# Performance work log

Hardware: AMD Instinct MI355X
Metric: run time of the kernel (lower is better)

## Reference

```python
import jax, jax.numpy as jnp
import numpy as np

H = 1024  # hidden_size
T = 64    # decode steps
B = 256
D_IN = 1024


def setup_inputs() -> dict:
    key = jax.random.key(0)
    ks = jax.random.split(key, 8)
    s = 0.05
    x = jax.random.normal(ks[0], (B, D_IN), dtype=jnp.float32)
    # first_state_dense: Dense(H, tanh)
    W_fs = jax.random.normal(ks[1], (D_IN, H), dtype=jnp.float32) * s
    b_fs = jnp.zeros((H,), dtype=jnp.float32)
    # output_dense: Dense(H, relu)
    W_out = jax.random.normal(ks[2], (H, H), dtype=jnp.float32) * s
    b_out = jnp.zeros((H,), dtype=jnp.float32)
    # Keras GRUCell (reset_after=True): kernel [H,3H], recurrent [H,3H], bias [2,3H]
    W_k = jax.random.normal(ks[3], (H, 3 * H), dtype=jnp.float32) * s
    W_r = jax.random.normal(ks[4], (H, 3 * H), dtype=jnp.float32) * s
    b_gru = jnp.zeros((2, 3 * H), dtype=jnp.float32)
    return {"x": x, "W_fs": W_fs, "b_fs": b_fs, "W_out": W_out,
            "b_out": b_out, "W_k": W_k, "W_r": W_r, "b_gru": b_gru}


def _gru_step(h, inp, W_k, W_r, b_gru):
    # Keras GRUCell math with reset_after=True (TF2 default)
    mx = inp @ W_k + b_gru[0]          # [B,3H]
    mh = h @ W_r + b_gru[1]            # [B,3H]
    xz, xr, xh = jnp.split(mx, 3, axis=-1)
    hz, hr, hh = jnp.split(mh, 3, axis=-1)
    z = jax.nn.sigmoid(xz + hz)
    r = jax.nn.sigmoid(xr + hr)
    hh_cand = jnp.tanh(xh + r * hh)
    return z * h + (1.0 - z) * hh_cand


def reference(x, W_fs, b_fs, W_out, b_out, W_k, W_r, b_gru):
    h0 = jnp.tanh(x @ W_fs + b_fs)  # [B,H]

    def step(h, _):
        out = jax.nn.relu(h @ W_out + b_out)   # [B,H]
        h_new = _gru_step(h, out, W_k, W_r, b_gru)
        return h_new, out

    h_final, outs = jax.lax.scan(step, h0, None, length=T)  # outs: [T,B,H]
    final_out = jax.nn.relu(h_final @ W_out + b_out)         # [B,H]
    # original collects T+1 outputs then drops the first
    collected = jnp.concatenate([outs[1:], final_out[None]], axis=0)  # [T,B,H]
    return jnp.transpose(collected, (1, 0, 2))  # [B,T,H]
```

## Files before the change

kernel.cpp:

```cpp
#include <hip/hip_runtime.h>
#include <math.h>

#define HDIM 1024
#define BROWS 256
#define TSTEPS 64
#define TH3 3072
#define RSCALE 1024.0f
#define RINV   0.0009765625f

typedef _Float16 half8 __attribute__((ext_vector_type(8)));
typedef float float4v __attribute__((ext_vector_type(4)));

__device__ __forceinline__ float sigmoidf_(float x) {
    return 1.0f / (1.0f + __expf(-x));
}

__device__ __forceinline__ float4v mfma16(half8 a, half8 b, float4v c) {
    return __builtin_amdgcn_mfma_f32_16x16x32_f16(a, b, c, 0, 0, 0);
}

__device__ __forceinline__ int frag_idx(int m, int k) {
    return (((m >> 4) * 32 + (k >> 5)) * 64 + ((m & 15) + (((k & 31) >> 3) << 4))) * 8 + (k & 7);
}

__device__ __forceinline__ void split16(float v, _Float16* hp, _Float16* lp) {
    const _Float16 h = (_Float16)v;
    *hp = h;
    *lp = (_Float16)((v - (float)h) * RSCALE);
}

__device__ __forceinline__ void st_h16(_Float16* p, _Float16 v) {
    const unsigned u = (unsigned)__builtin_bit_cast(unsigned short, v);
    asm volatile("global_store_short %0, %1, off sc0 sc1"
                 :: "v"(p), "v"(u) : "memory");
}

__device__ __forceinline__ void gbar_arrive(unsigned* bar, unsigned gen, bool isdes) {
    asm volatile("s_waitcnt vmcnt(0)" ::: "memory");
    __syncthreads();
    if (threadIdx.x == 0) {
        if (isdes) {
            asm volatile("buffer_inv sc0 sc1\n\ts_waitcnt vmcnt(0)" ::: "memory");
        } else {
            asm volatile("buffer_inv sc0\n\ts_waitcnt vmcnt(0)" ::: "memory");
        }
        unsigned* gc = bar + ((blockIdx.x & 7) << 5);
        unsigned* rc = bar + 256;
        const unsigned old = __hip_atomic_fetch_add(gc, 1u, __ATOMIC_RELAXED,
                                                    __HIP_MEMORY_SCOPE_AGENT);
        if (old + 1u == gen * 32u)
            __hip_atomic_fetch_add(rc, 1u, __ATOMIC_RELAXED,
                                   __HIP_MEMORY_SCOPE_AGENT);
    }
}

__device__ __forceinline__ void gbar_wait(unsigned* bar, unsigned gen) {
    if (threadIdx.x == 0) {
        unsigned* rc = bar + 256;
        while (__hip_atomic_load(rc, __ATOMIC_RELAXED,
                                 __HIP_MEMORY_SCOPE_AGENT) < gen * 8u)
            __builtin_amdgcn_s_sleep(1);
    }
    __syncthreads();
    asm volatile("" ::: "memory");
}

__device__ __forceinline__ void gbar(unsigned* bar, unsigned gen, bool isdes) {
    gbar_arrive(bar, gen, isdes);
    gbar_wait(bar, gen);
}

__device__ __forceinline__ void gbar_full(unsigned* bar, unsigned gen) {
    asm volatile("s_waitcnt vmcnt(0)" ::: "memory");
    __syncthreads();
    __builtin_amdgcn_fence(__ATOMIC_ACQUIRE, "agent");
    if (threadIdx.x == 0) {
        unsigned* gc = bar + ((blockIdx.x & 7) << 5);
        unsigned* rc = bar + 256;
        const unsigned old = __hip_atomic_fetch_add(gc, 1u, __ATOMIC_RELAXED,
                                                    __HIP_MEMORY_SCOPE_AGENT);
        if (old + 1u == gen * 32u)
            __hip_atomic_fetch_add(rc, 1u, __ATOMIC_RELAXED,
                                   __HIP_MEMORY_SCOPE_AGENT);
    }
    gbar_wait(bar, gen);
}

__device__ __forceinline__ void gemm_panel(
    const half8* __restrict__ AH, const half8* __restrict__ AL,
    const _Float16* __restrict__ WH, const _Float16* __restrict__ WL,
    int mt0, int mt1, int lane, int rot,
    float4v& aH0, float4v& aXa0, float4v& aXb0,
    float4v& aH1, float4v& aXa1, float4v& aXb1)
{
    half8 rA[2][2][4];
    const int base0 = mt0 * 2048 + lane;
    const int base1 = mt1 * 2048 + lane;
    const int lofs = lane * 8;
#pragma unroll
    for (int kk = 0; kk < 2; ++kk) {
        const int kt = (rot & 15) * 2 + kk;
        rA[0][kk][0] = AH[base0 + kt * 64];
        rA[0][kk][1] = AL[base0 + kt * 64];
        rA[0][kk][2] = AH[base1 + kt * 64];
        rA[0][kk][3] = AL[base1 + kt * 64];
    }
#pragma unroll
    for (int c = 0; c < 16; ++c) {
        if (c < 15) {
#pragma unroll
            for (int kk = 0; kk < 2; ++kk) {
                const int kt = (((c + 1) + rot) & 15) * 2 + kk;
                rA[(c + 1) & 1][kk][0] = AH[base0 + kt * 64];
                rA[(c + 1) & 1][kk][1] = AL[base0 + kt * 64];
                rA[(c + 1) & 1][kk][2] = AH[base1 + kt * 64];
                rA[(c + 1) & 1][kk][3] = AL[base1 + kt * 64];
            }
        }
#pragma unroll
        for (int kk = 0; kk < 2; ++kk) {
            const int kt = ((c + rot) & 15) * 2 + kk;
            const half8 bh = *(const half8*)&WH[kt * 512 + lofs];
            const half8 bl = *(const half8*)&WL[kt * 512 + lofs];
            const half8 a0h = rA[c & 1][kk][0];
            const half8 a0l = rA[c & 1][kk][1];
            const half8 a1h = rA[c & 1][kk][2];
            const half8 a1l = rA[c & 1][kk][3];
            aH0  = mfma16(a0h, bh, aH0);
            aXa0 = mfma16(a0l, bh, aXa0);
            aXb0 = mfma16(a0h, bl, aXb0);
            aH1  = mfma16(a1h, bh, aH1);
            aXa1 = mfma16(a1l, bh, aXa1);
            aXb1 = mfma16(a1h, bl, aXb1);
        }
    }
}

__global__ __launch_bounds__(512, 2) void decoder_mfma(
    const float* __restrict__ x,
    const float* __restrict__ W_fs, const float* __restrict__ b_fs,
    const float* __restrict__ W_out, const float* __restrict__ b_out,
    const float* __restrict__ W_k,  const float* __restrict__ W_r,
    const float* __restrict__ b_gru,
    float* __restrict__ dout,
    _Float16* __restrict__ hH, _Float16* __restrict__ hL,
    _Float16* __restrict__ oH, _Float16* __restrict__ oL,
    unsigned* __restrict__ bar)
{
    extern __shared__ _Float16 ldsh[];
    _Float16* WAh = ldsh;
    _Float16* WAl = ldsh + 16384;
    _Float16* WBh = ldsh + 32768;
    _Float16* WBl = ldsh + 49152;
    float*    mhs = (float*)(ldsh + 65536);
    volatile unsigned* peer_sh = (volatile unsigned*)(ldsh + 71680);

    const int b    = blockIdx.x;
    const int tid  = threadIdx.x;
    const int wv   = tid >> 6;
    const int lane = tid & 63;
    const int nn   = lane & 15;
    const int kq   = lane >> 4;

    unsigned xcd;
    asm("s_getreg_b32 %0, hwreg(HW_REG_XCC_ID)" : "=s"(xcd));
    xcd &= 7u;
    if (tid == 0) {
        __hip_atomic_fetch_max(&bar[288 + xcd], (unsigned)b, __ATOMIC_RELAXED,
                               __HIP_MEMORY_SCOPE_AGENT);
        peer_sh[0] = __hip_atomic_fetch_add(&bar[296 + xcd], 1u, __ATOMIC_RELAXED,
                                            __HIP_MEMORY_SCOPE_AGENT);
    }

    for (int idx = tid; idx < 16384; idx += 512) {
        const int k = idx >> 4, n = idx & 15;
        float w;
        if (n < 4) {
            w = W_out[(size_t)k * HDIM + 4 * b + n];
        } else {
            const int q = n - 4, jj = q / 3, ch = q - 3 * jj;
            w = W_r[(size_t)k * TH3 + ch * 1024 + 4 * b + jj];
        }
        const int hw = ((k >> 5) * 64 + n + (((k & 31) >> 3) << 4)) * 8 + (k & 7);
        split16(w, &WAh[hw], &WAl[hw]);
    }
    for (int idx = tid; idx < 16384; idx += 512) {
        const int k = idx >> 4, n = idx & 15;
        float w = 0.0f;
        if (n < 12) {
            const int jj = n / 3, ch = n - 3 * jj;
            w = W_k[(size_t)k * TH3 + ch * 1024 + 4 * b + jj];
        }
        const int hw = ((k >> 5) * 64 + n + (((k & 31) >> 3) << 4)) * 8 + (k & 7);
        split16(w, &WBh[hw], &WBl[hw]);
    }

    float bA;
    if (nn < 4) {
        bA = b_out[4 * b + nn];
    } else {
        const int q = nn - 4, jj = q / 3, ch = q - 3 * jj;
        bA = b_gru[TH3 + ch * 1024 + 4 * b + jj];
    }
    float bB = 0.0f;
    if (nn < 12) {
        const int jj = nn / 3, ch = nn - 3 * jj;
        bB = b_gru[ch * 1024 + 4 * b + jj];
    }

    {
        const int row = tid & 255;
        const int c = 4 * b + ((tid >> 8) << 1);
        float a0 = 0.0f, a1 = 0.0f;
        const float* xr = x + (size_t)row * HDIM;
        for (int k = 0; k < HDIM; k += 4) {
            const float4 xv = *(const float4*)(xr + k);
#pragma unroll
            for (int kk = 0; kk < 4; ++kk) {
                const float2 wv2 = *(const float2*)(W_fs + (size_t)(k + kk) * HDIM + c);
                const float av = (&xv.x)[kk];
                a0 = fmaf(av, wv2.x, a0);
                a1 = fmaf(av, wv2.y, a1);
            }
        }
        const float h0 = tanhf(a0 + b_fs[c]);
        const float h1 = tanhf(a1 + b_fs[c + 1]);
        _Float16 hi, lo;
        split16(h0, &hi, &lo);
        st_h16(&hH[frag_idx(row, c)], hi);
        st_h16(&hL[frag_idx(row, c)], lo);
        split16(h1, &hi, &lo);
        st_h16(&hH[frag_idx(row, c + 1)], hi);
        st_h16(&hL[frag_idx(row, c + 1)], lo);
    }
    unsigned gen = 0;
    gbar_full(bar, ++gen);

    const unsigned desblk = __hip_atomic_load(&bar[288 + xcd], __ATOMIC_RELAXED,
                                              __HIP_MEMORY_SCOPE_AGENT);
    const bool isdes = (desblk == (unsigned)b);
    const int p = (int)(peer_sh[0] & 31u);
    const int pair = (wv + (p & 7)) & 7;
    const int rot  = ((p >> 3) & 3) << 2;
    const int mt0 = 2 * pair, mt1 = 2 * pair + 1;
    float hreg[2][4];

    for (int t = 0; ; ++t) {
        {
            float4v aH0 = {0.f,0.f,0.f,0.f}, aXa0 = {0.f,0.f,0.f,0.f}, aXb0 = {0.f,0.f,0.f,0.f};
            float4v aH1 = {0.f,0.f,0.f,0.f}, aXa1 = {0.f,0.f,0.f,0.f}, aXb1 = {0.f,0.f,0.f,0.f};
            gemm_panel((const half8*)hH, (const half8*)hL, WAh, WAl,
                       mt0, mt1, lane, rot, aH0, aXa0, aXb0, aH1, aXa1, aXb1);
#pragma unroll
            for (int m = 0; m < 2; ++m) {
                const int mt = (m == 0) ? mt0 : mt1;
#pragma unroll
                for (int r = 0; r < 4; ++r) {
                    const int row = mt * 16 + kq * 4 + r;
                    float v = ((m == 0) ? aH0[r] + (aXa0[r] + aXb0[r]) * RINV
                                        : aH1[r] + (aXa1[r] + aXb1[r]) * RINV) + bA;
                    if (nn < 4) {
                        v = fmaxf(v, 0.0f);
                        if (t < TSTEPS) {
                            _Float16 hi, lo;
                            split16(v, &hi, &lo);
                            const int fi = frag_idx(row, 4 * b + nn);
                            st_h16(&oH[fi], hi);
                            st_h16(&oL[fi], lo);
                        }
                    } else if (t < TSTEPS) {
                        mhs[row * 12 + (nn - 4)] = v;
                    }
                }
            }
            if (t == TSTEPS) {
                if (nn < 4) {
#pragma unroll
                    for (int m = 0; m < 2; ++m) {
                        const int mt = (m == 0) ? mt0 : mt1;
#pragma unroll
                        for (int r = 0; r < 4; ++r) {
                            const int row = mt * 16 + kq * 4 + r;
                            const float v = fmaxf(((m == 0) ? aH0[r] + (aXa0[r] + aXb0[r]) * RINV
                                                            : aH1[r] + (aXa1[r] + aXb1[r]) * RINV) + bA, 0.0f);
                            __builtin_nontemporal_store(
                                v, &dout[(size_t)row * (TSTEPS * HDIM) +
                                         (size_t)(TSTEPS - 1) * HDIM + 4 * b + nn]);
                        }
                    }
                }
                break;
            }
            gbar_arrive(bar, ++gen, isdes);
            if (nn < 4 && t >= 1) {
#pragma unroll
                for (int m = 0; m < 2; ++m) {
                    const int mt = (m == 0) ? mt0 : mt1;
#pragma unroll
                    for (int r = 0; r < 4; ++r) {
                        const int row = mt * 16 + kq * 4 + r;
                        const float v = fmaxf(((m == 0) ? aH0[r] + (aXa0[r] + aXb0[r]) * RINV
                                                        : aH1[r] + (aXa1[r] + aXb1[r]) * RINV) + bA, 0.0f);
                        __builtin_nontemporal_store(
                            v, &dout[(size_t)row * (TSTEPS * HDIM) +
                                     (size_t)(t - 1) * HDIM + 4 * b + nn]);
                    }
                }
            }
            gbar_wait(bar, gen);
        }

        {
            float4v aH0 = {0.f,0.f,0.f,0.f}, aXa0 = {0.f,0.f,0.f,0.f}, aXb0 = {0.f,0.f,0.f,0.f};
            float4v aH1 = {0.f,0.f,0.f,0.f}, aXa1 = {0.f,0.f,0.f,0.f}, aXb1 = {0.f,0.f,0.f,0.f};
            gemm_panel((const half8*)oH, (const half8*)oL, WBh, WBl,
                       mt0, mt1, lane, rot, aH0, aXa0, aXb0, aH1, aXa1, aXb1);
            float vals[2][4], v1[2][4], v2[2][4];
#pragma unroll
            for (int r = 0; r < 4; ++r) {
                vals[0][r] = aH0[r] + (aXa0[r] + aXb0[r]) * RINV + bB;
                vals[1][r] = aH1[r] + (aXa1[r] + aXb1[r]) * RINV + bB;
            }
#pragma unroll
            for (int m = 0; m < 2; ++m)
#pragma unroll
                for (int r = 0; r < 4; ++r) {
                    v1[m][r] = __shfl(vals[m][r], (lane + 1) & 63);
                    v2[m][r] = __shfl(vals[m][r], (lane + 2) & 63);
                }
            if (nn < 12 && (nn % 3) == 0) {
                const int jj = nn / 3;
                const int j = 4 * b + jj;
                if (t == 0) {
#pragma unroll
                    for (int m = 0; m < 2; ++m)
#pragma unroll
                        for (int r = 0; r < 4; ++r) {
                            const int mt = (m == 0) ? mt0 : mt1;
                            const int row = mt * 16 + kq * 4 + r;
                            const int fi = frag_idx(row, j);
                            hreg[m][r] = (float)hH[fi] + (float)hL[fi] * RINV;
                        }
                }
#pragma unroll
                for (int m = 0; m < 2; ++m) {
                    const int mt = (m == 0) ? mt0 : mt1;
#pragma unroll
                    for (int r = 0; r < 4; ++r) {
                        const int row = mt * 16 + kq * 4 + r;
                        const float* mrow = &mhs[row * 12 + 3 * jj];
                        const float z    = sigmoidf_(vals[m][r] + mrow[0]);
                        const float rg   = sigmoidf_(v1[m][r] + mrow[1]);
                        const float cand = tanhf(v2[m][r] + rg * mrow[2]);
                        const float hn = z * hreg[m][r] + (1.0f - z) * cand;
                        hreg[m][r] = hn;
                        const int fi = frag_idx(row, j);
                        _Float16 hi, lo;
                        split16(hn, &hi, &lo);
                        st_h16(&hH[fi], hi);
                        st_h16(&hL[fi], lo);
                    }
                }
            }
            gbar(bar, ++gen, isdes);
        }
    }
}

__global__ __launch_bounds__(128) void gemmA(
    const float* __restrict__ A,
    const float* __restrict__ W0, const float* __restrict__ b0, int act0,
    float* __restrict__ C0, float* __restrict__ C2,
    const float* __restrict__ W1, const float* __restrict__ b1,
    float* __restrict__ C1)
{
    __shared__ __align__(16) float Ass[32][36];
    __shared__ __align__(16) float Ws[32][68];
    const int tid = threadIdx.x;
    const int bx = blockIdx.x, by = blockIdx.y;
    const int r0 = by * 32;
    const bool reg0 = (bx < 16);
    const int c0 = reg0 ? bx * 64 : (bx - 16) * 64;
    const float* __restrict__ W = reg0 ? W0 : W1;
    const int ldw = reg0 ? 1024 : 3072;
    const int arow = tid >> 2;
    const int ak   = (tid & 3) << 2;
    const int wrow = tid >> 4;
    const int wcol = (tid & 15) << 2;
    const int ty = tid >> 4;
    const int tx = tid & 15;
    float acc[4][4] = {};
    const float* Ap = A + (size_t)(r0 + arow) * 1024 + ak;
    const float* Wp = W + (size_t)wrow * ldw + c0 + wcol;
    for (int k0 = 0; k0 < 1024; k0 += 32) {
        const float4 a0 = *(const float4*)(Ap + k0);
        const float4 a1 = *(const float4*)(Ap + k0 + 16);
        const float4 w0 = *(const float4*)(Wp + (size_t)k0 * ldw);
        const float4 w1 = *(const float4*)(Wp + (size_t)(k0 + 8) * ldw);
        const float4 w2 = *(const float4*)(Wp + (size_t)(k0 + 16) * ldw);
        const float4 w3 = *(const float4*)(Wp + (size_t)(k0 + 24) * ldw);
        __syncthreads();
        Ass[ak + 0][arow] = a0.x; Ass[ak + 1][arow] = a0.y;
        Ass[ak + 2][arow] = a0.z; Ass[ak + 3][arow] = a0.w;
        Ass[ak + 16][arow] = a1.x; Ass[ak + 17][arow] = a1.y;
        Ass[ak + 18][arow] = a1.z; Ass[ak + 19][arow] = a1.w;
        *(float4*)&Ws[wrow][wcol]      = w0;
        *(float4*)&Ws[wrow + 8][wcol]  = w1;
        *(float4*)&Ws[wrow + 16][wcol] = w2;
        *(float4*)&Ws[wrow + 24][wcol] = w3;
        __syncthreads();
#pragma unroll
        for (int kk = 0; kk < 32; ++kk) {
            const float4 a4 = *(const float4*)&Ass[kk][ty << 2];
            const float4 w4 = *(const float4*)&Ws[kk][tx << 2];
            const float a[4] = {a4.x, a4.y, a4.z, a4.w};
            const float w[4] = {w4.x, w4.y, w4.z, w4.w};
#pragma unroll
            for (int i = 0; i < 4; ++i)
#pragma unroll
                for (int j = 0; j < 4; ++j)
                    acc[i][j] = fmaf(a[i], w[j], acc[i][j]);
        }
    }
    const float* bias = reg0 ? b0 : b1;
    const float4 bv = *(const float4*)(bias + c0 + (tx << 2));
    const float bb[4] = {bv.x, bv.y, bv.z, bv.w};
#pragma unroll
    for (int i = 0; i < 4; ++i) {
        const int row = r0 + (ty << 2) + i;
        float v[4];
#pragma unroll
        for (int j = 0; j < 4; ++j) {
            float tv = acc[i][j] + bb[j];
            if (reg0) { tv = (act0 == 1) ? fmaxf(tv, 0.0f) : tanhf(tv); }
            v[j] = tv;
        }
        const float4 o = make_float4(v[0], v[1], v[2], v[3]);
        if (reg0) {
            *(float4*)(C0 + (size_t)row * 1024 + c0 + (tx << 2)) = o;
            if (C2)
                *(float4*)(C2 + (size_t)row * (TSTEPS * HDIM) + c0 + (tx << 2)) = o;
        } else {
            *(float4*)(C1 + (size_t)row * TH3 + c0 + (tx << 2)) = o;
        }
    }
}

__global__ __launch_bounds__(128) void gemmB(
    const float* __restrict__ A,
    const float* __restrict__ Wk,
    const float* __restrict__ bg,
    const float* __restrict__ mh,
    float* __restrict__ h)
{
    __shared__ __align__(16) float Ass[32][36];
    __shared__ __align__(16) float Ws[3][32][20];
    const int tid = threadIdx.x;
    const int j0 = blockIdx.x * 16;
    const int r0 = blockIdx.y * 32;
    const int arow = tid >> 2;
    const int ak   = (tid & 3) << 2;
    const int wr   = tid >> 2;
    const int wc   = (tid & 3) << 2;
    const int ty = tid >> 4;
    const int tx = tid & 15;
    float acc[3][4] = {};
    const float* Ap = A + (size_t)(r0 + arow) * 1024 + ak;
    const float* Wp = Wk + (size_t)wr * TH3 + j0 + wc;
    for (int k0 = 0; k0 < 1024; k0 += 32) {
        const float4 a0 = *(const float4*)(Ap + k0);
        const float4 a1 = *(const float4*)(Ap + k0 + 16);
        float4 wv[3];
#pragma unroll
        for (int c = 0; c < 3; ++c)
            wv[c] = *(const float4*)(Wp + (size_t)k0 * TH3 + c * 1024);
        __syncthreads();
        Ass[ak + 0][arow] = a0.x; Ass[ak + 1][arow] = a0.y;
        Ass[ak + 2][arow] = a0.z; Ass[ak + 3][arow] = a0.w;
        Ass[ak + 16][arow] = a1.x; Ass[ak + 17][arow] = a1.y;
        Ass[ak + 18][arow] = a1.z; Ass[ak + 19][arow] = a1.w;
#pragma unroll
        for (int c = 0; c < 3; ++c)
            *(float4*)&Ws[c][wr][wc] = wv[c];
        __syncthreads();
#pragma unroll
        for (int kk = 0; kk < 32; ++kk) {
            const float4 a4 = *(const float4*)&Ass[kk][ty << 2];
            const float a[4] = {a4.x, a4.y, a4.z, a4.w};
            const float wz = Ws[0][kk][tx];
            const float wr_ = Ws[1][kk][tx];
            const float wh = Ws[2][kk][tx];
#pragma unroll
            for (int i = 0; i < 4; ++i) {
                acc[0][i] = fmaf(a[i], wz, acc[0][i]);
                acc[1][i] = fmaf(a[i], wr_, acc[1][i]);
                acc[2][i] = fmaf(a[i], wh, acc[2][i]);
            }
        }
    }
    const int j = j0 + tx;
    const float bz = bg[j];
    const float br = bg[HDIM + j];
    const float bh = bg[2 * HDIM + j];
#pragma unroll
    for (int i = 0; i < 4; ++i) {
        const int row = r0 + (ty << 2) + i;
        const float* mhp = mh + (size_t)row * TH3;
        const float z  = sigmoidf_(acc[0][i] + bz + mhp[j]);
        const float rg = sigmoidf_(acc[1][i] + br + mhp[HDIM + j]);
        const float cand = tanhf(acc[2][i] + bh + rg * mhp[2 * HDIM + j]);
        const size_t hi = (size_t)row * HDIM + j;
        const float ho = h[hi];
        h[hi] = z * ho + (1.0f - z) * cand;
    }
}

extern "C" void kernel_launch(void* const* d_in, const int* in_sizes, int n_in,
                              void* d_out, int out_size, void* d_ws, size_t ws_size,
                              hipStream_t stream) {
    const float* x     = (const float*)d_in[0];
    const float* W_fs  = (const float*)d_in[1];
    const float* b_fs  = (const float*)d_in[2];
    const float* W_out = (const float*)d_in[3];
    const float* b_out = (const float*)d_in[4];
    const float* W_k   = (const float*)d_in[5];
    const float* W_r   = (const float*)d_in[6];
    const float* b_gru = (const float*)d_in[7];
    float* out = (float*)d_out;

    char* ws = (char*)d_ws;
    _Float16* hH = (_Float16*)(ws);
    _Float16* hL = (_Float16*)(ws + 512 * 1024);
    _Float16* oH = (_Float16*)(ws + 1024 * 1024);
    _Float16* oL = (_Float16*)(ws + 1536 * 1024);
    unsigned* bar = (unsigned*)(ws + 2048 * 1024);

    hipMemsetAsync(bar, 0, 2048, stream);

    void* args[] = {
        (void*)&x, (void*)&W_fs, (void*)&b_fs, (void*)&W_out, (void*)&b_out,
        (void*)&W_k, (void*)&W_r, (void*)&b_gru, (void*)&out,
        (void*)&hH, (void*)&hL, (void*)&oH, (void*)&oL, (void*)&bar
    };
    const size_t lds_bytes = 131072 + 12288 + 256;
    hipError_t err = hipLaunchCooperativeKernel(
        (const void*)decoder_mfma, dim3(256), dim3(512),
        args, lds_bytes, stream);

    if (err != hipSuccess) {
        float* h    = (float*)d_ws;
        float* outb = h    + BROWS * HDIM;
        float* mhf  = outb + BROWS * HDIM;
        const dim3 blk(128);
        const dim3 gridInit(16, 8);
        const dim3 gridA(64, 8);
        const dim3 gridB(64, 8);
        gemmA<<<gridInit, blk, 0, stream>>>(x, W_fs, b_fs, 2, h, nullptr,
                                            nullptr, nullptr, nullptr);
        for (int t = 0; t < TSTEPS; ++t) {
            float* c2 = (t >= 1) ? (out + (size_t)(t - 1) * HDIM) : nullptr;
            gemmA<<<gridA, blk, 0, stream>>>(h, W_out, b_out, 1, outb, c2,
                                             W_r, b_gru + TH3, mhf);
            gemmB<<<gridB, blk, 0, stream>>>(outb, W_k, b_gru, mhf, h);
        }
        gemmA<<<gridInit, blk, 0, stream>>>(h, W_out, b_out, 1, outb,
                                            out + (size_t)(TSTEPS - 1) * HDIM,
                                            nullptr, nullptr, nullptr);
    }
}
```

Before: 3.960 ms.

## Prefetch activation panel into per-XCD L2 by designated block before GEMM

```diff
diff --git a/kernel.cpp b/kernel.cpp
--- a/kernel.cpp
+++ b/kernel.cpp
@@ -84,6 +84,34 @@
                                    __HIP_MEMORY_SCOPE_AGENT);
     }
     gbar_wait(bar, gen);
+}
+
+__device__ __forceinline__ void sweep1MB(const char* base, int tid) {
+    float a = 0.0f;
+#pragma unroll
+    for (int j = 0; j < 16; ++j)
+        a += *(const float*)(base + (size_t)(((j << 9) | tid) << 7));
+    asm volatile("" :: "v"(a));
+}
+
+__device__ __forceinline__ void flag_set(unsigned* bar, unsigned xcd, unsigned fg) {
+    asm volatile("s_waitcnt vmcnt(0)" ::: "memory");
+    __syncthreads();
+    if (threadIdx.x == 0)
+        __hip_atomic_store(&bar[304 + xcd], fg, __ATOMIC_RELAXED,
+                           __HIP_MEMORY_SCOPE_AGENT);
+}
+
+__device__ __forceinline__ void flag_wait(unsigned* bar, unsigned xcd, unsigned fg) {
+    if (threadIdx.x == 0) {
+        int tries = 0;
+        while (__hip_atomic_load(&bar[304 + xcd], __ATOMIC_RELAXED,
+                                 __HIP_MEMORY_SCOPE_AGENT) < fg) {
+            __builtin_amdgcn_s_sleep(2);
+            if (++tries > 4096) break;
+        }
+    }
+    __syncthreads();
 }
 
 __device__ __forceinline__ void gemm_panel(
@@ -240,13 +268,17 @@
                                               __HIP_MEMORY_SCOPE_AGENT);
     const bool isdes = (desblk == (unsigned)b);
     const int p = (int)(peer_sh[0] & 31u);
-    const int pair = (wv + (p & 7)) & 7;
-    const int rot  = ((p >> 3) & 3) << 2;
-    const int mt0 = 2 * pair, mt1 = 2 * pair + 1;
+    const int rot = p & 15;
+    const int mt0 = 2 * wv, mt1 = 2 * wv + 1;
     float hreg[2][4];
+    unsigned fg = 0;
 
     for (int t = 0; ; ++t) {
         {
+            ++fg;
+            if (isdes) { sweep1MB((const char*)hH, tid); flag_set(bar, xcd, fg); }
+            else       { flag_wait(bar, xcd, fg); }
+
             float4v aH0 = {0.f,0.f,0.f,0.f}, aXa0 = {0.f,0.f,0.f,0.f}, aXb0 = {0.f,0.f,0.f,0.f};
             float4v aH1 = {0.f,0.f,0.f,0.f}, aXa1 = {0.f,0.f,0.f,0.f}, aXb1 = {0.f,0.f,0.f,0.f};
             gemm_panel((const half8*)hH, (const half8*)hL, WAh, WAl,
@@ -311,6 +343,10 @@
         }
 
         {
+            ++fg;
+            if (isdes) { sweep1MB((const char*)oH, tid); flag_set(bar, xcd, fg); }
+            else       { flag_wait(bar, xcd, fg); }
+
             float4v aH0 = {0.f,0.f,0.f,0.f}, aXa0 = {0.f,0.f,0.f,0.f}, aXb0 = {0.f,0.f,0.f,0.f};
             float4v aH1 = {0.f,0.f,0.f,0.f}, aXa1 = {0.f,0.f,0.f,0.f}, aXb1 = {0.f,0.f,0.f,0.f};
             gemm_panel((const half8*)oH, (const half8*)oL, WBh, WBl,
```

Result: slower. 5.312 ms (+34.1%).

## Use per-XCD release slot in grid barrier and simplify row-tile mapping

Applied to the files above, without the earlier changes.

```diff
diff --git a/kernel.cpp b/kernel.cpp
--- a/kernel.cpp
+++ b/kernel.cpp
@@ -35,55 +35,85 @@
                  :: "v"(p), "v"(u) : "memory");
 }
 
-__device__ __forceinline__ void gbar_arrive(unsigned* bar, unsigned gen, bool isdes) {
+__device__ __forceinline__ bool gbar_arrive(unsigned* bar, unsigned gen,
+                                            bool isdes, unsigned xcd) {
     asm volatile("s_waitcnt vmcnt(0)" ::: "memory");
     __syncthreads();
+    bool last = false;
     if (threadIdx.x == 0) {
         if (isdes) {
             asm volatile("buffer_inv sc0 sc1\n\ts_waitcnt vmcnt(0)" ::: "memory");
         } else {
             asm volatile("buffer_inv sc0\n\ts_waitcnt vmcnt(0)" ::: "memory");
         }
-        unsigned* gc = bar + ((blockIdx.x & 7) << 5);
+        unsigned* gc = bar + (xcd << 5);
+        unsigned* rc = bar + 256;
+        const unsigned old = __hip_atomic_fetch_add(gc, 1u, __ATOMIC_RELAXED,
+                                                    __HIP_MEMORY_SCOPE_AGENT);
+        if (old + 1u == gen * 32u) {
+            __hip_atomic_fetch_add(rc, 1u, __ATOMIC_RELAXED,
+                                   __HIP_MEMORY_SCOPE_AGENT);
+            last = true;
+        }
+    }
+    return last;
+}
+
+__device__ __forceinline__ void gbar_wait(unsigned* bar, unsigned gen,
+                                          bool last, unsigned xcd) {
+    if (threadIdx.x == 0) {
+        unsigned* rc = bar + 256;
+        unsigned* slot = bar + 320 + xcd * 16;
+        if (last) {
+            while (__hip_atomic_load(rc, __ATOMIC_RELAXED,
+                                     __HIP_MEMORY_SCOPE_AGENT) < gen * 8u)
+                __builtin_amdgcn_s_sleep(1);
+            asm volatile("global_store_dword %0, %1, off sc0"
+                         :: "v"(slot), "v"(gen) : "memory");
+        } else {
+            int it = 0;
+            for (;;) {
+                unsigned v;
+                asm volatile("global_load_dword %0, %1, off sc0\n\t"
+                             "s_waitcnt vmcnt(0)"
+                             : "=v"(v) : "v"(slot) : "memory");
+                if (v >= gen) break;
+                if ((++it & 31) == 0 &&
+                    __hip_atomic_load(rc, __ATOMIC_RELAXED,
+                                      __HIP_MEMORY_SCOPE_AGENT) >= gen * 8u)
+                    break;
+                __builtin_amdgcn_s_sleep(2);
+            }
+        }
+    }
+    __syncthreads();
+    asm volatile("" ::: "memory");
+}
+
+__device__ __forceinline__ void gbar(unsigned* bar, unsigned gen,
+                                     bool isdes, unsigned xcd) {
+    const bool last = gbar_arrive(bar, gen, isdes, xcd);
+    gbar_wait(bar, gen, last, xcd);
+}
+
+__device__ __forceinline__ void gbar_full(unsigned* bar, unsigned gen, unsigned xcd) {
+    asm volatile("s_waitcnt vmcnt(0)" ::: "memory");
+    __syncthreads();
+    __builtin_amdgcn_fence(__ATOMIC_ACQUIRE, "agent");
+    if (threadIdx.x == 0) {
+        unsigned* gc = bar + (xcd << 5);
         unsigned* rc = bar + 256;
         const unsigned old = __hip_atomic_fetch_add(gc, 1u, __ATOMIC_RELAXED,
                                                     __HIP_MEMORY_SCOPE_AGENT);
         if (old + 1u == gen * 32u)
             __hip_atomic_fetch_add(rc, 1u, __ATOMIC_RELAXED,
                                    __HIP_MEMORY_SCOPE_AGENT);
-    }
-}
-
-__device__ __forceinline__ void gbar_wait(unsigned* bar, unsigned gen) {
-    if (threadIdx.x == 0) {
-        unsigned* rc = bar + 256;
         while (__hip_atomic_load(rc, __ATOMIC_RELAXED,
                                  __HIP_MEMORY_SCOPE_AGENT) < gen * 8u)
             __builtin_amdgcn_s_sleep(1);
     }
     __syncthreads();
     asm volatile("" ::: "memory");
-}
-
-__device__ __forceinline__ void gbar(unsigned* bar, unsigned gen, bool isdes) {
-    gbar_arrive(bar, gen, isdes);
-    gbar_wait(bar, gen);
-}
-
-__device__ __forceinline__ void gbar_full(unsigned* bar, unsigned gen) {
-    asm volatile("s_waitcnt vmcnt(0)" ::: "memory");
-    __syncthreads();
-    __builtin_amdgcn_fence(__ATOMIC_ACQUIRE, "agent");
-    if (threadIdx.x == 0) {
-        unsigned* gc = bar + ((blockIdx.x & 7) << 5);
-        unsigned* rc = bar + 256;
-        const unsigned old = __hip_atomic_fetch_add(gc, 1u, __ATOMIC_RELAXED,
-                                                    __HIP_MEMORY_SCOPE_AGENT);
-        if (old + 1u == gen * 32u)
-            __hip_atomic_fetch_add(rc, 1u, __ATOMIC_RELAXED,
-                                   __HIP_MEMORY_SCOPE_AGENT);
-    }
-    gbar_wait(bar, gen);
 }
 
 __device__ __forceinline__ void gemm_panel(
@@ -234,15 +264,14 @@
         st_h16(&hL[frag_idx(row, c + 1)], lo);
     }
     unsigned gen = 0;
-    gbar_full(bar, ++gen);
+    gbar_full(bar, ++gen, xcd);
 
     const unsigned desblk = __hip_atomic_load(&bar[288 + xcd], __ATOMIC_RELAXED,
                                               __HIP_MEMORY_SCOPE_AGENT);
     const bool isdes = (desblk == (unsigned)b);
     const int p = (int)(peer_sh[0] & 31u);
-    const int pair = (wv + (p & 7)) & 7;
-    const int rot  = ((p >> 3) & 3) << 2;
-    const int mt0 = 2 * pair, mt1 = 2 * pair + 1;
+    const int rot = p & 15;
+    const int mt0 = 2 * wv, mt1 = 2 * wv + 1;
     float hreg[2][4];
 
     for (int t = 0; ; ++t) {
@@ -291,7 +320,7 @@
                 }
                 break;
             }
-            gbar_arrive(bar, ++gen, isdes);
+            const bool last = gbar_arrive(bar, ++gen, isdes, xcd);
             if (nn < 4 && t >= 1) {
 #pragma unroll
                 for (int m = 0; m < 2; ++m) {
@@ -307,7 +336,7 @@
                     }
                 }
             }
-            gbar_wait(bar, gen);
+            gbar_wait(bar, gen, last, xcd);
         }
 
         {
@@ -362,7 +391,7 @@
                     }
                 }
             }
-            gbar(bar, ++gen, isdes);
+            gbar(bar, ++gen, isdes, xcd);
         }
     }
 }
```

Measured after the change: 4.234 ms. 6.9% more time.
